# Optimization experiments

Measured on AMD Instinct MI355X. Metric: run time of the kernel, lower is better.

The kernel has to match this reference:

```python
import jax, jax.numpy as jnp
import numpy as np

NUM_HEADS = 32
NUM_KV_HEADS = 8
HEAD_DIM = 128
HIDDEN = 4096
B, L = 2, 4096


def _phi(x):
    # feature map: elu(x) + 1
    return jax.nn.elu(x) + 1.0


def setup_inputs() -> dict:
    key = jax.random.key(0)
    ks = jax.random.split(key, 9)
    s = 1.0 / np.sqrt(HIDDEN)
    return {
        "hidden_states": jax.random.normal(ks[0], (B, L, HIDDEN), jnp.float32),
        "Wq": jax.random.normal(ks[1], (HIDDEN, HIDDEN), jnp.float32) * s,
        "bq": jnp.zeros((HIDDEN,), jnp.float32),
        "Wk": jax.random.normal(ks[2], (NUM_KV_HEADS * HEAD_DIM, HIDDEN), jnp.float32) * s,
        "bk": jnp.zeros((NUM_KV_HEADS * HEAD_DIM,), jnp.float32),
        "Wv": jax.random.normal(ks[3], (NUM_KV_HEADS * HEAD_DIM, HIDDEN), jnp.float32) * s,
        "bv": jnp.zeros((NUM_KV_HEADS * HEAD_DIM,), jnp.float32),
        "Wo": jax.random.normal(ks[4], (HIDDEN, HIDDEN), jnp.float32) * s,
        "bo": jnp.zeros((HIDDEN,), jnp.float32),
    }


def reference(hidden_states, Wq, bq, Wk, bk, Wv, bv, Wo, bo):
    bsz, q_len, _ = hidden_states.shape
    n_rep = NUM_HEADS // NUM_KV_HEADS

    # projections (nn.Linear: y = x @ W.T + b)
    q = hidden_states @ Wq.T + bq          # [B, L, H*D]
    k = hidden_states @ Wk.T + bk          # [B, L, Hkv*D]
    v = hidden_states @ Wv.T + bv

    q = q.reshape(bsz, q_len, NUM_HEADS, HEAD_DIM).transpose(0, 2, 1, 3)       # [B,H,L,D]
    k = k.reshape(bsz, q_len, NUM_KV_HEADS, HEAD_DIM).transpose(0, 2, 1, 3)    # [B,Hkv,L,D]
    v = v.reshape(bsz, q_len, NUM_KV_HEADS, HEAD_DIM).transpose(0, 2, 1, 3)

    # repeat_kv: [B,Hkv,L,D] -> [B,H,L,D]
    k = jnp.broadcast_to(k[:, :, None], (bsz, NUM_KV_HEADS, n_rep, q_len, HEAD_DIM)).reshape(bsz, NUM_HEADS, q_len, HEAD_DIM)
    v = jnp.broadcast_to(v[:, :, None], (bsz, NUM_KV_HEADS, n_rep, q_len, HEAD_DIM)).reshape(bsz, NUM_HEADS, q_len, HEAD_DIM)

    q = _phi(q)
    k = _phi(k)

    # global KV summary: O(L*d^2) linear attention
    key_value = jnp.einsum('bhld,bhlv->bhvd', k, v)           # [B,H,D,D]
    attn = jnp.einsum('bhqd,bhvd->bhqv', q, key_value)        # [B,H,L,D]

    # normalizer: sum of feature-mapped keys over sequence, per channel
    normalizer = k.sum(axis=2)[:, :, None, :]                  # [B,H,1,D]
    attn = attn / (normalizer + 1e-10)

    attn = attn.transpose(0, 2, 1, 3).reshape(bsz, q_len, HIDDEN)
    return attn @ Wo.T + bo
```

## Files before the change

kernel.cpp:

```cpp
#include <hip/hip_runtime.h>

#define HIDDEN 4096
#define NKV 8
#define NH 32
#define HD 128
#define BATCH 2
#define SEQ 4096
#define ROWS (BATCH*SEQ)

typedef short bf16x8 __attribute__((ext_vector_type(8)));
typedef float f32x4 __attribute__((ext_vector_type(4)));

static __device__ __forceinline__ float bf2f(unsigned short u) {
    union { unsigned int i; float f; } c; c.i = ((unsigned int)u) << 16; return c.f;
}
static __device__ __forceinline__ unsigned short f2bf(float x) {
    union { float f; unsigned int i; } c; c.f = x;
    unsigned int r = c.i + 0x7fffu + ((c.i >> 16) & 1u);
    return (unsigned short)(r >> 16);
}

static __device__ __forceinline__ void gl2lds16(const void* g, void* l) {
    __builtin_amdgcn_global_load_lds(
        (const __attribute__((address_space(1))) unsigned int*)g,
        (__attribute__((address_space(3))) unsigned int*)l, 16, 0, 0);
}

#define WGBAR() __builtin_amdgcn_s_barrier()
#define VMW(n) asm volatile("s_waitcnt vmcnt(" #n ")" ::: "memory")
#define LGKM(n) asm volatile("s_waitcnt lgkmcnt(" #n ")" ::: "memory")
#define SCHED_FENCE() __builtin_amdgcn_sched_barrier(0)

__global__ __launch_bounds__(256)
void cast_kernel(const float* __restrict__ in, unsigned short* __restrict__ out, int n4) {
    int idx = blockIdx.x * blockDim.x + threadIdx.x;
    int stride = gridDim.x * blockDim.x;
    for (int i = idx; i < n4; i += stride) {
        float4 f = ((const float4*)in)[i];
        ushort4 o;
        o.x = f2bf(f.x); o.y = f2bf(f.y); o.z = f2bf(f.z); o.w = f2bf(f.w);
        ((ushort4*)out)[i] = o;
    }
}

template<int MODE>
__global__ __launch_bounds__(512, 2)
void gemm256(const unsigned short* __restrict__ A, int lda,
             const unsigned short* __restrict__ B, int ldb,
             const float* __restrict__ bias0, const float* __restrict__ bias1,
             void* __restrict__ Cout, int M, int N, int K)
{
    __shared__ __align__(16) unsigned char sm[131072];

    const int tid = threadIdx.x;
    const int wid = tid >> 6, lane = tid & 63;
    const int wr = wid >> 2, wc = wid & 3;
    const int lr = lane & 15, kg = lane >> 4;
    const int lswz = (lane & 7) << 4;

    int nbx = N >> 8;
    int nwg = nbx * (M >> 8);
    int cpx = nwg >> 3;
    int bid = (int)blockIdx.x;
    int wg = (bid & 7) * cpx + (bid >> 3);
    int bx = wg % nbx, by = wg / nbx;
    int rowBase = by << 8, colBase = bx << 8;

    size_t sA[2][2], sB[2][2];
#pragma unroll
    for (int h = 0; h < 2; ++h)
#pragma unroll
        for (int i = 0; i < 2; ++i) {
            int o = i * 8192 + wid * 1024 + lane * 16;
            int row = o >> 7;
            int ce = ((o & 127) ^ ((row & 7) << 4)) >> 1;
            sA[h][i] = (size_t)(rowBase + h * 128 + row) * lda + ce;
            sB[h][i] = (size_t)(colBase + h * 128 + row) * ldb + ce;
        }
    const int ldsW = wid * 1024;

    auto SA = [&](int nb, int h, int i, size_t ko) {
        gl2lds16(A + sA[h][i] + ko, sm + nb + h * 16384 + i * 8192 + ldsW);
    };
    auto SB = [&](int nb, int h, int i, size_t ko) {
        gl2lds16(B + sB[h][i] + ko, sm + nb + 32768 + h * 16384 + i * 8192 + ldsW);
    };
    auto STAGE = [&](int buf, size_t ko) {
        int nb = buf << 16;
        SB(nb, 0, 0, ko); SB(nb, 0, 1, ko); SB(nb, 1, 0, ko); SB(nb, 1, 1, ko);
        SA(nb, 0, 0, ko); SA(nb, 1, 0, ko); SA(nb, 0, 1, ko); SA(nb, 1, 1, ko);
    };

    const int aRd = wr * 16384 + (lr << 7);
    const int bRd = 32768 + (wc >> 1) * 16384 + (((wc & 1) * 64 + lr) << 7);
    const int kcol0 = (kg * 16) ^ lswz;
    const int kcol1 = (64 + kg * 16) ^ lswz;

    auto RA = [&](int cb, int mp, int ks) -> bf16x8 {
        return *(const bf16x8*)(sm + cb + aRd + mp * 2048 + (ks ? kcol1 : kcol0));
    };
    auto RB = [&](int cb, int n, int ks) -> bf16x8 {
        return *(const bf16x8*)(sm + cb + bRd + n * 2048 + (ks ? kcol1 : kcol0));
    };

    f32x4 acc[8][4] = {};
    bf16x8 bfr[4][2];

    auto MF = [&](bf16x8 a0, bf16x8 a1, bf16x8 a2, bf16x8 a3, int m0, int m1) {
        SCHED_FENCE();
        __builtin_amdgcn_s_setprio(1);
#pragma unroll
        for (int n = 0; n < 4; ++n) {
            acc[m0][n] = __builtin_amdgcn_mfma_f32_16x16x32_bf16(a0, bfr[n][0], acc[m0][n], 0, 0, 0);
            acc[m0][n] = __builtin_amdgcn_mfma_f32_16x16x32_bf16(a1, bfr[n][1], acc[m0][n], 0, 0, 0);
            acc[m1][n] = __builtin_amdgcn_mfma_f32_16x16x32_bf16(a2, bfr[n][0], acc[m1][n], 0, 0, 0);
            acc[m1][n] = __builtin_amdgcn_mfma_f32_16x16x32_bf16(a3, bfr[n][1], acc[m1][n], 0, 0, 0);
        }
        __builtin_amdgcn_s_setprio(0);
    };

    const int NT = K >> 6;

    STAGE(0, 0);
    VMW(0);
    WGBAR();
    SCHED_FENCE();

    int cur = 0;
    for (int t = 0; t < NT; ++t) {
        const int cb = cur << 16;
        if (t + 1 < NT) {
            STAGE(cur ^ 1, (size_t)(t + 1) * 64);
        }
        bf16x8 a0 = RA(cb, 0, 0), a1 = RA(cb, 0, 1), a2 = RA(cb, 1, 0), a3 = RA(cb, 1, 1);
#pragma unroll
        for (int n = 0; n < 4; ++n) { bfr[n][0] = RB(cb, n, 0); bfr[n][1] = RB(cb, n, 1); }
        bf16x8 b0 = RA(cb, 2, 0), b1 = RA(cb, 2, 1), b2 = RA(cb, 3, 0), b3 = RA(cb, 3, 1);
        LGKM(4);
        MF(a0, a1, a2, a3, 0, 1);
        a0 = RA(cb, 4, 0); a1 = RA(cb, 4, 1); a2 = RA(cb, 5, 0); a3 = RA(cb, 5, 1);
        LGKM(4);
        MF(b0, b1, b2, b3, 2, 3);
        b0 = RA(cb, 6, 0); b1 = RA(cb, 6, 1); b2 = RA(cb, 7, 0); b3 = RA(cb, 7, 1);
        LGKM(4);
        MF(a0, a1, a2, a3, 4, 5);
        LGKM(0);
        MF(b0, b1, b2, b3, 6, 7);
        if (t + 1 < NT) {
            VMW(0);
            WGBAR();
            SCHED_FENCE();
        }
        cur ^= 1;
    }

    int r0 = rowBase + wr * 128 + kg * 4;
    int c0 = colBase + wc * 64 + lr;
#pragma unroll
    for (int n = 0; n < 4; ++n) {
        int col = c0 + n * 16;
        float bv;
        if (MODE == 2) bv = (col < 1024) ? bias0[col] : bias1[col - 1024];
        else           bv = bias0[col];
#pragma unroll
        for (int m = 0; m < 8; ++m) {
            int row = r0 + m * 16;
#pragma unroll
            for (int r = 0; r < 4; ++r) {
                float v = acc[m][n][r] + bv;
                if (MODE == 1) v = (v > 0.f) ? v + 1.f : __expf(v);
                if (MODE == 2 && col < 1024) v = (v > 0.f) ? v + 1.f : __expf(v);
                if (MODE == 0) ((float*)Cout)[(size_t)(row + r) * N + col] = v;
                else ((unsigned short*)Cout)[(size_t)(row + r) * N + col] = f2bf(v);
            }
        }
    }
}

__global__ __launch_bounds__(256)
void kv_partial(const unsigned short* __restrict__ Kb, const unsigned short* __restrict__ Vb,
                int ld, float* __restrict__ kvp, float* __restrict__ ksp)
{
    int chunk = blockIdx.x;
    int g = blockIdx.y;
    int b = g >> 3, hkv = g & 7;
    __shared__ float kl[32][128];
    __shared__ float vl[32][128];
    int tid = threadIdx.x;
    int c0 = (tid >> 4) * 8, d0 = (tid & 15) * 8;
    float acc[8][8] = {};
    float ksacc = 0.0f;
    size_t rowBase = (size_t)b * SEQ + (size_t)chunk * 128;

    for (int sch = 0; sch < 4; ++sch) {
        __syncthreads();
        for (int t = tid; t < 512; t += 256) {
            int l = t >> 4, col = (t & 15) * 8;
            size_t off = (rowBase + sch * 32 + l) * ld + hkv * HD + col;
            uint4 kr = *(const uint4*)(Kb + off);
            uint4 vr = *(const uint4*)(Vb + off);
            unsigned int ku[4] = {kr.x, kr.y, kr.z, kr.w};
            unsigned int vu[4] = {vr.x, vr.y, vr.z, vr.w};
#pragma unroll
            for (int q = 0; q < 4; ++q) {
                kl[l][col + q * 2]     = bf2f((unsigned short)(ku[q] & 0xffff));
                kl[l][col + q * 2 + 1] = bf2f((unsigned short)(ku[q] >> 16));
                vl[l][col + q * 2]     = bf2f((unsigned short)(vu[q] & 0xffff));
                vl[l][col + q * 2 + 1] = bf2f((unsigned short)(vu[q] >> 16));
            }
        }
        __syncthreads();
        for (int l = 0; l < 32; ++l) {
            float vv[8], kk[8];
#pragma unroll
            for (int x = 0; x < 8; ++x) { vv[x] = vl[l][c0 + x]; kk[x] = kl[l][d0 + x]; }
#pragma unroll
            for (int x = 0; x < 8; ++x)
#pragma unroll
                for (int y = 0; y < 8; ++y)
                    acc[x][y] += vv[x] * kk[y];
        }
        if (tid < 128) {
            for (int l = 0; l < 32; ++l) ksacc += kl[l][tid];
        }
    }
    float* out = kvp + ((size_t)g * 32 + chunk) * (HD * HD);
#pragma unroll
    for (int x = 0; x < 8; ++x)
#pragma unroll
        for (int y = 0; y < 8; ++y)
            out[(c0 + x) * HD + d0 + y] = acc[x][y];
    if (tid < 128) ksp[((size_t)g * 32 + chunk) * HD + tid] = ksacc;
}

__global__ __launch_bounds__(256)
void kv_reduce(const float* __restrict__ kvp, const float* __restrict__ ksp,
               unsigned short* __restrict__ kvb, float* __restrict__ ksum)
{
    int slice = blockIdx.x;
    int g = blockIdx.y;
    int tid = threadIdx.x;
    int e = slice * 1024 + tid * 4;
    float4 s = {0.f, 0.f, 0.f, 0.f};
    for (int ch = 0; ch < 32; ++ch) {
        float4 p = *(const float4*)(kvp + ((size_t)g * 32 + ch) * (HD * HD) + e);
        s.x += p.x; s.y += p.y; s.z += p.z; s.w += p.w;
    }
    ushort4 o;
    o.x = f2bf(s.x); o.y = f2bf(s.y); o.z = f2bf(s.z); o.w = f2bf(s.w);
    *(ushort4*)(kvb + (size_t)g * HD * HD + e) = o;
    if (slice == 0 && tid < 128) {
        float ss = 0.f;
        for (int ch = 0; ch < 32; ++ch) ss += ksp[((size_t)g * 32 + ch) * HD + tid];
        ksum[g * HD + tid] = ss;
    }
}

__global__ __launch_bounds__(256)
void attn_gemm(const unsigned short* __restrict__ Q,
               const unsigned short* __restrict__ KV,
               const float* __restrict__ KS,
               unsigned short* __restrict__ Out)
{
    const int BK = 32;
    __shared__ unsigned short As[128 * BK];
    __shared__ unsigned short Bs[128 * BK];

    int rt = blockIdx.x;
    int h  = blockIdx.y;
    int g = (rt >> 5) * NKV + (h >> 2);
    int rowBase = rt << 7;

    const unsigned short* A = Q + (size_t)h * HD;
    const unsigned short* B = KV + (size_t)g * HD * HD;
    const float* ks = KS + g * HD;

    int tid = threadIdx.x;
    int wave = tid >> 6, lane = tid & 63;
    int wr = wave >> 1, wc = wave & 1;

    f32x4 acc[4][4] = {};

    int sr = lane >> 2;
    int sc = (lane & 3) * 8;

    const unsigned short* Aw = A + (size_t)(rowBase + wave * 32 + sr) * HIDDEN + sc;
    const unsigned short* Bw = B + (size_t)(wave * 32 + sr) * HD + sc;
    unsigned short* Asw = As + wave * 32 * BK;
    unsigned short* Bsw = Bs + wave * 32 * BK;

    int arow = (wr * 64 + (lane & 15)) * BK + (lane >> 4) * 8;
    int brow = (wc * 64 + (lane & 15)) * BK + (lane >> 4) * 8;

    for (int kt = 0; kt < HD; kt += BK) {
        gl2lds16(Aw + kt, Asw);
        gl2lds16(Aw + kt + (size_t)16 * HIDDEN, Asw + 16 * BK);
        gl2lds16(Bw + kt, Bsw);
        gl2lds16(Bw + kt + (size_t)16 * HD, Bsw + 16 * BK);
        __syncthreads();
        bf16x8 af[4], bfr[4];
#pragma unroll
        for (int i = 0; i < 4; ++i) af[i] = *(const bf16x8*)&As[arow + i * 16 * BK];
#pragma unroll
        for (int j = 0; j < 4; ++j) bfr[j] = *(const bf16x8*)&Bs[brow + j * 16 * BK];
#pragma unroll
        for (int i = 0; i < 4; ++i)
#pragma unroll
            for (int j = 0; j < 4; ++j)
                acc[i][j] = __builtin_amdgcn_mfma_f32_16x16x32_bf16(af[i], bfr[j], acc[i][j], 0, 0, 0);
        __syncthreads();
    }

    int r0 = rowBase + wr * 64 + ((lane >> 4) << 2);
    int c0 = wc * 64 + (lane & 15);
#pragma unroll
    for (int j = 0; j < 4; ++j) {
        int col = c0 + j * 16;
        float inv = 1.0f / (ks[col] + 1e-10f);
#pragma unroll
        for (int i = 0; i < 4; ++i) {
            int row = r0 + i * 16;
#pragma unroll
            for (int r = 0; r < 4; ++r) {
                float v = acc[i][j][r] * inv;
                Out[(size_t)(row + r) * HIDDEN + h * HD + col] = f2bf(v);
            }
        }
    }
}

extern "C" void kernel_launch(void* const* d_in, const int* in_sizes, int n_in,
                              void* d_out, int out_size, void* d_ws, size_t ws_size,
                              hipStream_t stream)
{
    const float* hs = (const float*)d_in[0];
    const float* Wq = (const float*)d_in[1];
    const float* bq = (const float*)d_in[2];
    const float* Wk = (const float*)d_in[3];
    const float* bk = (const float*)d_in[4];
    const float* Wv = (const float*)d_in[5];
    const float* bv = (const float*)d_in[6];
    const float* Wo = (const float*)d_in[7];
    const float* bo = (const float*)d_in[8];

    char* ws = (char*)d_ws;
    size_t off = 0;
    auto alloc = [&](size_t bytes) -> char* {
        char* p = ws + off;
        off += (bytes + 255) & ~(size_t)255;
        return p;
    };

    unsigned short* hs_b  = (unsigned short*)alloc((size_t)ROWS * HIDDEN * 2);
    unsigned short* Wq_b  = (unsigned short*)alloc((size_t)HIDDEN * HIDDEN * 2);
    unsigned short* Wkv_b = (unsigned short*)alloc((size_t)2048 * HIDDEN * 2);
    unsigned short* Wo_b  = (unsigned short*)alloc((size_t)HIDDEN * HIDDEN * 2);
    unsigned short* kvout = (unsigned short*)alloc((size_t)ROWS * 2048 * 2);
    float* ksp   = (float*)alloc((size_t)16 * 32 * HD * 4);
    unsigned short* kvb = (unsigned short*)alloc((size_t)16 * HD * HD * 2);
    float* ksum  = (float*)alloc((size_t)16 * HD * 4);

    float* kvp = (float*)Wq_b;
    unsigned short* attn_b = hs_b;
    unsigned short* q_b = (unsigned short*)d_out;

    (void)in_sizes; (void)n_in; (void)out_size; (void)ws_size;

    auto cast = [&](const float* in, unsigned short* out, size_t n) {
        int n4 = (int)(n / 4);
        int blocks = (n4 + 255) / 256;
        if (blocks > 2048) blocks = 2048;
        cast_kernel<<<dim3(blocks), dim3(256), 0, stream>>>(in, out, n4);
    };

    cast(hs, hs_b, (size_t)ROWS * HIDDEN);
    cast(Wq, Wq_b, (size_t)HIDDEN * HIDDEN);
    cast(Wk, Wkv_b, (size_t)1024 * HIDDEN);
    cast(Wv, Wkv_b + (size_t)1024 * HIDDEN, (size_t)1024 * HIDDEN);
    cast(Wo, Wo_b, (size_t)HIDDEN * HIDDEN);

    gemm256<1><<<dim3(512), dim3(512), 0, stream>>>(hs_b, HIDDEN, Wq_b, HIDDEN, bq, nullptr, q_b, ROWS, HIDDEN, HIDDEN);
    gemm256<2><<<dim3(256), dim3(512), 0, stream>>>(hs_b, HIDDEN, Wkv_b, HIDDEN, bk, bv, kvout, ROWS, 2048, HIDDEN);

    kv_partial<<<dim3(32, 16), dim3(256), 0, stream>>>(kvout, kvout + 1024, 2048, kvp, ksp);
    kv_reduce<<<dim3(16, 16), dim3(256), 0, stream>>>(kvp, ksp, kvb, ksum);

    attn_gemm<<<dim3(64, 32), dim3(256), 0, stream>>>(q_b, kvb, ksum, attn_b);

    gemm256<0><<<dim3(512), dim3(512), 0, stream>>>(attn_b, HIDDEN, Wo_b, HIDDEN, bo, nullptr, d_out, ROWS, HIDDEN, HIDDEN);
}
```

Before: 772.7 us.

## Merge five cast launches into one and drop manual MFMA scheduling hints

Replaces five separate fp32-to-bf16 cast launches with a single kernel that walks a segment table, removing launch overhead and the tail of each small launch. Separately, the GEMM inner loop drops its explicit lgkmcnt waits, sched_barrier fences and s_setprio calls, leaving LDS-read and MFMA interleaving to the compiler. Letting the compiler insert waits may produce more conservative or different scheduling, and dropping the priority hints can change how waves overlap.

New measurement: 760.1 us. No clear change (-1.6%).

```diff
diff --git a/kernel.cpp b/kernel.cpp
--- a/kernel.cpp
+++ b/kernel.cpp
@@ -28,18 +28,31 @@
 
 #define WGBAR() __builtin_amdgcn_s_barrier()
 #define VMW(n) asm volatile("s_waitcnt vmcnt(" #n ")" ::: "memory")
-#define LGKM(n) asm volatile("s_waitcnt lgkmcnt(" #n ")" ::: "memory")
 #define SCHED_FENCE() __builtin_amdgcn_sched_barrier(0)
 
+struct CastSegs {
+    const float* in[5];
+    unsigned short* out[5];
+    int n4[5];
+    int cum[5];
+    int total;
+};
+
 __global__ __launch_bounds__(256)
-void cast_kernel(const float* __restrict__ in, unsigned short* __restrict__ out, int n4) {
+void cast5_kernel(CastSegs s) {
     int idx = blockIdx.x * blockDim.x + threadIdx.x;
     int stride = gridDim.x * blockDim.x;
-    for (int i = idx; i < n4; i += stride) {
-        float4 f = ((const float4*)in)[i];
+    for (int i = idx; i < s.total; i += stride) {
+        int seg = 0;
+        if (i >= s.cum[1]) seg = 1;
+        if (i >= s.cum[2]) seg = 2;
+        if (i >= s.cum[3]) seg = 3;
+        if (i >= s.cum[4]) seg = 4;
+        int j = i - s.cum[seg];
+        float4 f = ((const float4*)s.in[seg])[j];
         ushort4 o;
         o.x = f2bf(f.x); o.y = f2bf(f.y); o.z = f2bf(f.z); o.w = f2bf(f.w);
-        ((ushort4*)out)[i] = o;
+        ((ushort4*)s.out[seg])[j] = o;
     }
 }
 
@@ -107,8 +120,6 @@
     bf16x8 bfr[4][2];
 
     auto MF = [&](bf16x8 a0, bf16x8 a1, bf16x8 a2, bf16x8 a3, int m0, int m1) {
-        SCHED_FENCE();
-        __builtin_amdgcn_s_setprio(1);
 #pragma unroll
         for (int n = 0; n < 4; ++n) {
             acc[m0][n] = __builtin_amdgcn_mfma_f32_16x16x32_bf16(a0, bfr[n][0], acc[m0][n], 0, 0, 0);
@@ -116,7 +127,6 @@
             acc[m1][n] = __builtin_amdgcn_mfma_f32_16x16x32_bf16(a2, bfr[n][0], acc[m1][n], 0, 0, 0);
             acc[m1][n] = __builtin_amdgcn_mfma_f32_16x16x32_bf16(a3, bfr[n][1], acc[m1][n], 0, 0, 0);
         }
-        __builtin_amdgcn_s_setprio(0);
     };
 
     const int NT = K >> 6;
@@ -136,15 +146,11 @@
 #pragma unroll
         for (int n = 0; n < 4; ++n) { bfr[n][0] = RB(cb, n, 0); bfr[n][1] = RB(cb, n, 1); }
         bf16x8 b0 = RA(cb, 2, 0), b1 = RA(cb, 2, 1), b2 = RA(cb, 3, 0), b3 = RA(cb, 3, 1);
-        LGKM(4);
         MF(a0, a1, a2, a3, 0, 1);
         a0 = RA(cb, 4, 0); a1 = RA(cb, 4, 1); a2 = RA(cb, 5, 0); a3 = RA(cb, 5, 1);
-        LGKM(4);
         MF(b0, b1, b2, b3, 2, 3);
         b0 = RA(cb, 6, 0); b1 = RA(cb, 6, 1); b2 = RA(cb, 7, 0); b3 = RA(cb, 7, 1);
-        LGKM(4);
         MF(a0, a1, a2, a3, 4, 5);
-        LGKM(0);
         MF(b0, b1, b2, b3, 6, 7);
         if (t + 1 < NT) {
             VMW(0);
@@ -366,18 +372,16 @@
 
     (void)in_sizes; (void)n_in; (void)out_size; (void)ws_size;
 
-    auto cast = [&](const float* in, unsigned short* out, size_t n) {
-        int n4 = (int)(n / 4);
-        int blocks = (n4 + 255) / 256;
-        if (blocks > 2048) blocks = 2048;
-        cast_kernel<<<dim3(blocks), dim3(256), 0, stream>>>(in, out, n4);
-    };
-
-    cast(hs, hs_b, (size_t)ROWS * HIDDEN);
-    cast(Wq, Wq_b, (size_t)HIDDEN * HIDDEN);
-    cast(Wk, Wkv_b, (size_t)1024 * HIDDEN);
-    cast(Wv, Wkv_b + (size_t)1024 * HIDDEN, (size_t)1024 * HIDDEN);
-    cast(Wo, Wo_b, (size_t)HIDDEN * HIDDEN);
+    CastSegs cs;
+    cs.in[0] = hs;  cs.out[0] = hs_b;                         cs.n4[0] = (ROWS * HIDDEN) / 4;
+    cs.in[1] = Wq;  cs.out[1] = Wq_b;                         cs.n4[1] = (HIDDEN * HIDDEN) / 4;
+    cs.in[2] = Wk;  cs.out[2] = Wkv_b;                        cs.n4[2] = (1024 * HIDDEN) / 4;
+    cs.in[3] = Wv;  cs.out[3] = Wkv_b + (size_t)1024 * HIDDEN; cs.n4[3] = (1024 * HIDDEN) / 4;
+    cs.in[4] = Wo;  cs.out[4] = Wo_b;                         cs.n4[4] = (HIDDEN * HIDDEN) / 4;
+    cs.cum[0] = 0;
+    for (int i = 1; i < 5; ++i) cs.cum[i] = cs.cum[i - 1] + cs.n4[i - 1];
+    cs.total = cs.cum[4] + cs.n4[4];
+    cast5_kernel<<<dim3(2048), dim3(256), 0, stream>>>(cs);
 
     gemm256<1><<<dim3(512), dim3(512), 0, stream>>>(hs_b, HIDDEN, Wq_b, HIDDEN, bq, nullptr, q_b, ROWS, HIDDEN, HIDDEN);
     gemm256<2><<<dim3(256), dim3(512), 0, stream>>>(hs_b, HIDDEN, Wkv_b, HIDDEN, bk, bv, kvout, ROWS, 2048, HIDDEN);
```
